# Kernel tuning notes

Hardware: AMD Instinct MI355X
Metric: run time of the kernel (lower is better)

The kernel has to match this reference:

```python
import jax, jax.numpy as jnp
import numpy as np

N, D = 8192, 128

def setup_inputs() -> dict:
    key = jax.random.key(0)
    kF, kS = jax.random.split(key)
    F = jax.random.normal(kF, (N, D), dtype=jnp.float32)
    S = jax.random.uniform(kS, (N, N), dtype=jnp.float32)
    return {"F": F, "S": S, "t": 1, "T": 10}

def reference(F, S, t, T):
    # Pairwise squared euclidean distances via Gram trick:
    # D_ij = ||f_i||^2 + ||f_j||^2 - 2 f_i . f_j  (same math as norm(F[:,None]-F)^2)
    sq = jnp.sum(F * F, axis=1)                      # [N]
    dist2 = sq[:, None] + sq[None, :] - 2.0 * (F @ F.T)  # [N, N]
    # select=False: loss = sum over i of sum_j dist2[i,j] * S[i,j]
    loss = jnp.sum(dist2 * S)
    return loss
```

## Files before the change

kernel.cpp:

```cpp
#include <hip/hip_runtime.h>

#define NN 8192
#define DD 128
#define BM 128
#define NTILE (NN / BM)

typedef __attribute__((ext_vector_type(8))) short bf16x8;
typedef __attribute__((ext_vector_type(4))) float f32x4;

__device__ __forceinline__ ushort f2bf(float x) {
    unsigned u = __float_as_uint(x);
    unsigned r = u + 0x7FFFu + ((u >> 16) & 1u);
    return (ushort)(r >> 16);
}

__device__ __forceinline__ void async16(void* lds, const void* g) {
    __builtin_amdgcn_global_load_lds(
        (const __attribute__((address_space(1))) unsigned*)g,
        (__attribute__((address_space(3))) unsigned*)lds, 16, 0, 0);
}
__device__ __forceinline__ void async4(void* lds, const void* g) {
    __builtin_amdgcn_global_load_lds(
        (const __attribute__((address_space(1))) unsigned*)g,
        (__attribute__((address_space(3))) unsigned*)lds, 4, 0, 0);
}

__global__ void prep_kernel(const float* __restrict__ F, ushort* __restrict__ Fbf,
                            float* __restrict__ sq, int doFbf) {
    int gtid = blockIdx.x * blockDim.x + threadIdx.x;
    int row  = gtid >> 6;
    int lane = threadIdx.x & 63;
    const float2 v = *(const float2*)(F + (size_t)row * DD + lane * 2);
    if (doFbf)
        ((ushort2*)(Fbf + (size_t)row * DD))[lane] = make_ushort2(f2bf(v.x), f2bf(v.y));
    float s = v.x * v.x + v.y * v.y;
    #pragma unroll
    for (int off = 32; off > 0; off >>= 1) s += __shfl_down(s, off);
    if (lane == 0) sq[row] = s;
}

template <int FAST>
__global__ __launch_bounds__(256, 2) void tile_kernel(
        const ushort* __restrict__ Fbf, const float* __restrict__ F,
        const float* __restrict__ S, const float* __restrict__ sq,
        float* __restrict__ partials) {
    __shared__ ushort lI[BM * DD];
    __shared__ ushort lJ[BM * DD];
    __shared__ float  sqi[BM];
    __shared__ float  sqj[BM];
    __shared__ float  red[4];

    const int bi = blockIdx.y, bj = blockIdx.x;
    const int gi = bi * BM, gj = bj * BM;
    const int tid = threadIdx.x;
    const int w = tid >> 6, l = tid & 63;

    if (FAST) {
        #pragma unroll
        for (int it = 0; it < 8; ++it) {
            const int chunk = it * 4 + w;
            const int row = chunk * 4 + (l >> 4);
            const int inb = (l & 15) * 16;
            const int src = inb ^ ((row & 7) << 4);
            async16((char*)lI + chunk * 1024, (const char*)(Fbf + (size_t)(gi + row) * DD) + src);
            async16((char*)lJ + chunk * 1024, (const char*)(Fbf + (size_t)(gj + row) * DD) + src);
        }
        {
            float* dstb = (w < 2 ? sqi : sqj) + (w & 1) * 64;
            const float* srcb = sq + (w < 2 ? gi : gj) + (w & 1) * 64 + l;
            async4(dstb, srcb);
        }
    } else {
        const int r0 = tid >> 5;
        const int c4 = (tid & 31) * 4;
        #pragma unroll
        for (int it = 0; it < 16; ++it) {
            const int row = it * 8 + r0;
            const float4 va = *(const float4*)(F + (size_t)(gi + row) * DD + c4);
            const float4 vb = *(const float4*)(F + (size_t)(gj + row) * DD + c4);
            int byte = row * 256 + c4 * 2;
            byte ^= (row & 7) << 4;
            *(ushort4*)((char*)lI + byte) =
                make_ushort4(f2bf(va.x), f2bf(va.y), f2bf(va.z), f2bf(va.w));
            *(ushort4*)((char*)lJ + byte) =
                make_ushort4(f2bf(vb.x), f2bf(vb.y), f2bf(vb.z), f2bf(vb.w));
        }
        if (tid < 128) sqi[tid] = sq[gi + tid];
        else           sqj[tid - 128] = sq[gj + tid - 128];
    }
    __syncthreads();

    const int fr = l & 15;
    const int g  = l >> 4;
    const int jw = w * 32;

    float4 sv0[8], sv1[8];
    #pragma unroll
    for (int ct = 0; ct < 8; ++ct) {
        const float* srow = S + (size_t)(gi + ct * 16 + fr) * NN + gj + jw + g * 4;
        sv0[ct] = *(const float4*)(srow);
        sv1[ct] = *(const float4*)(srow + 16);
    }

    bf16x8 afrag[2][4];
    #pragma unroll
    for (int kk = 0; kk < 4; ++kk) {
        {
            const int row = jw + fr;
            int byte = row * 256 + kk * 64 + g * 16;
            byte ^= (row & 7) << 4;
            afrag[0][kk] = *(const bf16x8*)((const char*)lJ + byte);
        }
        {
            const int row = jw + 16 + fr;
            int byte = row * 256 + kk * 64 + g * 16;
            byte ^= (row & 7) << 4;
            afrag[1][kk] = *(const bf16x8*)((const char*)lJ + byte);
        }
    }

    f32x4 acc[2][8];
    #pragma unroll
    for (int ct = 0; ct < 8; ++ct) {
        acc[0][ct] = (f32x4){0.f, 0.f, 0.f, 0.f};
        acc[1][ct] = (f32x4){0.f, 0.f, 0.f, 0.f};
    }

    #pragma unroll
    for (int ct = 0; ct < 8; ++ct) {
        #pragma unroll
        for (int kk = 0; kk < 4; ++kk) {
            const int row = ct * 16 + fr;
            int byte = row * 256 + kk * 64 + g * 16;
            byte ^= (row & 7) << 4;
            const bf16x8 bfrag = *(const bf16x8*)((const char*)lI + byte);
            acc[0][ct] = __builtin_amdgcn_mfma_f32_16x16x32_bf16(
                afrag[0][kk], bfrag, acc[0][ct], 0, 0, 0);
            acc[1][ct] = __builtin_amdgcn_mfma_f32_16x16x32_bf16(
                afrag[1][kk], bfrag, acc[1][ct], 0, 0, 0);
        }
    }

    const float4 sj0 = *(const float4*)(sqj + jw + g * 4);
    const float4 sj1 = *(const float4*)(sqj + jw + 16 + g * 4);
    float part = 0.f;
    #pragma unroll
    for (int ct = 0; ct < 8; ++ct) {
        const float si = sqi[ct * 16 + fr];
        const float4 s0 = sv0[ct], s1 = sv1[ct];
        part += s0.x * (si + sj0.x - 2.f * acc[0][ct][0]);
        part += s0.y * (si + sj0.y - 2.f * acc[0][ct][1]);
        part += s0.z * (si + sj0.z - 2.f * acc[0][ct][2]);
        part += s0.w * (si + sj0.w - 2.f * acc[0][ct][3]);
        part += s1.x * (si + sj1.x - 2.f * acc[1][ct][0]);
        part += s1.y * (si + sj1.y - 2.f * acc[1][ct][1]);
        part += s1.z * (si + sj1.z - 2.f * acc[1][ct][2]);
        part += s1.w * (si + sj1.w - 2.f * acc[1][ct][3]);
    }

    #pragma unroll
    for (int off = 32; off > 0; off >>= 1) part += __shfl_down(part, off);
    if (l == 0) red[w] = part;
    __syncthreads();
    if (tid == 0)
        partials[blockIdx.y * gridDim.x + blockIdx.x] = (red[0] + red[1]) + (red[2] + red[3]);
}

__global__ void reduce_kernel(const float* __restrict__ partials, float* __restrict__ out) {
    __shared__ float sm[256];
    const int t = threadIdx.x;
    float s = 0.f;
    for (int i = t; i < NTILE * NTILE; i += 256) s += partials[i];
    sm[t] = s;
    __syncthreads();
    for (int off = 128; off > 0; off >>= 1) {
        if (t < off) sm[t] += sm[t + off];
        __syncthreads();
    }
    if (t == 0) out[0] = sm[0];
}

extern "C" void kernel_launch(void* const* d_in, const int* in_sizes, int n_in,
                              void* d_out, int out_size, void* d_ws, size_t ws_size,
                              hipStream_t stream) {
    const float* F = (const float*)d_in[0];
    const float* S = (const float*)d_in[1];
    float* sq       = (float*)d_ws;
    float* partials = sq + NN;
    ushort* Fbf     = (ushort*)((char*)d_ws + 48 * 1024);
    float* out      = (float*)d_out;

    const size_t need = 48 * 1024 + (size_t)NN * DD * 2 + 256;
    const int fast = (ws_size >= need) ? 1 : 0;

    prep_kernel<<<NN / 4, 256, 0, stream>>>(F, Fbf, sq, fast);
    dim3 grid(NTILE, NTILE);
    if (fast)
        tile_kernel<1><<<grid, 256, 0, stream>>>(Fbf, F, S, sq, partials);
    else
        tile_kernel<0><<<grid, 256, 0, stream>>>(Fbf, F, S, sq, partials);
    reduce_kernel<<<1, 256, 0, stream>>>(partials, out);
}
```

Baseline: 69.13 us.

## Persistent row-block loop with double-buffered J tiles and fused final reduction

Replaces the one-tile-per-block grid with 256 blocks of 512 threads, each looping over 16 column tiles for a fixed row block. The I tile stays resident in LDS while the next J tile (via async global-to-LDS loads) and its S values are prefetched into double buffers during the MFMA work on the current tile. The separate reduce kernel is dropped in favour of an atomic-counter last-block reduction, removing one launch. The cost is more registers and LDS per block, hand-tuned waitcnt values that must match the number of outstanding loads, and only 256 blocks to spread across the CUs.

```diff
diff --git a/kernel.cpp b/kernel.cpp
--- a/kernel.cpp
+++ b/kernel.cpp
@@ -3,6 +3,7 @@
 #define NN 8192
 #define DD 128
 #define BM 128
+#define NT 16
 #define NTILE (NN / BM)
 
 typedef __attribute__((ext_vector_type(8))) short bf16x8;
@@ -19,14 +20,10 @@
         (const __attribute__((address_space(1))) unsigned*)g,
         (__attribute__((address_space(3))) unsigned*)lds, 16, 0, 0);
 }
-__device__ __forceinline__ void async4(void* lds, const void* g) {
-    __builtin_amdgcn_global_load_lds(
-        (const __attribute__((address_space(1))) unsigned*)g,
-        (__attribute__((address_space(3))) unsigned*)lds, 4, 0, 0);
-}
 
 __global__ void prep_kernel(const float* __restrict__ F, ushort* __restrict__ Fbf,
-                            float* __restrict__ sq, int doFbf) {
+                            float* __restrict__ sq, int* counter, int doFbf) {
+    if (blockIdx.x == 0 && threadIdx.x == 0 && counter) *counter = 0;
     int gtid = blockIdx.x * blockDim.x + threadIdx.x;
     int row  = gtid >> 6;
     int lane = threadIdx.x & 63;
@@ -39,11 +36,143 @@
     if (lane == 0) sq[row] = s;
 }
 
-template <int FAST>
-__global__ __launch_bounds__(256, 2) void tile_kernel(
-        const ushort* __restrict__ Fbf, const float* __restrict__ F,
-        const float* __restrict__ S, const float* __restrict__ sq,
-        float* __restrict__ partials) {
+#define BODY(T, SVC, SJC, SVN, SJN, RBUF, WBUF)                               \
+  {                                                                           \
+    const int t_ = (T);                                                       \
+    if (t_ < NT - 1) {                                                        \
+      const int jr0 = jg0 + (t_ + 1) * BM;                                    \
+      _Pragma("unroll")                                                       \
+      for (int it = 0; it < 4; ++it) {                                        \
+        const int c = it * 8 + w;                                             \
+        const int row = c * 4 + (l >> 4);                                     \
+        const int src = ((l & 15) * 16) ^ ((row & 7) << 4);                   \
+        async16((char*)(WBUF) + c * 1024,                                     \
+                (const char*)(Fbf + (size_t)(jr0 + row) * DD) + src);         \
+      }                                                                       \
+      __builtin_amdgcn_sched_barrier(0);                                      \
+      const float* sb_ = sbase + jr0;                                         \
+      _Pragma("unroll")                                                       \
+      for (int ct = 0; ct < 8; ++ct)                                          \
+        SVN[ct] = *(const float4*)(sb_ + (size_t)ct * 16 * NN);               \
+      SJN = *(const float4*)(sq + jr0 + jcol);                                \
+      __builtin_amdgcn_sched_barrier(0);                                      \
+    }                                                                         \
+    bf16x8 af[4];                                                             \
+    {                                                                         \
+      const int row = jw + fr;                                                \
+      const int sw = (row & 7) << 4;                                          \
+      _Pragma("unroll")                                                       \
+      for (int kk = 0; kk < 4; ++kk)                                          \
+        af[kk] = *(const bf16x8*)((const char*)RBUF + row * 256 +             \
+                                  ((kk * 64 + g * 16) ^ sw));                 \
+    }                                                                         \
+    f32x4 acc[8];                                                             \
+    _Pragma("unroll")                                                         \
+    for (int ct = 0; ct < 8; ++ct) acc[ct] = (f32x4){0.f, 0.f, 0.f, 0.f};     \
+    _Pragma("unroll")                                                         \
+    for (int ct = 0; ct < 8; ++ct) {                                          \
+      const int row = ct * 16 + fr;                                           \
+      const int sw = (row & 7) << 4;                                          \
+      _Pragma("unroll")                                                       \
+      for (int kk = 0; kk < 4; ++kk) {                                        \
+        const bf16x8 bf_ = *(const bf16x8*)((const char*)lI + row * 256 +     \
+                                            ((kk * 64 + g * 16) ^ sw));       \
+        acc[ct] = __builtin_amdgcn_mfma_f32_16x16x32_bf16(af[kk], bf_,        \
+                                                          acc[ct], 0, 0, 0);  \
+      }                                                                       \
+    }                                                                         \
+    _Pragma("unroll")                                                         \
+    for (int ct = 0; ct < 8; ++ct) {                                          \
+      const float4 s4 = SVC[ct];                                              \
+      const float c0 = si[ct] + SJC.x, c1 = si[ct] + SJC.y,                   \
+                  c2 = si[ct] + SJC.z, c3 = si[ct] + SJC.w;                   \
+      part0 += s4.x * (c0 - 2.f * acc[ct][0]);                                \
+      part1 += s4.y * (c1 - 2.f * acc[ct][1]);                                \
+      part0 += s4.z * (c2 - 2.f * acc[ct][2]);                                \
+      part1 += s4.w * (c3 - 2.f * acc[ct][3]);                                \
+    }                                                                         \
+    if (t_ < NT - 1) {                                                        \
+      asm volatile("s_waitcnt vmcnt(9)" ::: "memory");                        \
+      __builtin_amdgcn_sched_barrier(0);                                      \
+      __builtin_amdgcn_s_barrier();                                           \
+    }                                                                         \
+  }
+
+__global__ __launch_bounds__(512, 2) void tile_loop_kernel(
+        const ushort* __restrict__ Fbf, const float* __restrict__ S,
+        const float* __restrict__ sq, float* __restrict__ partials,
+        int* __restrict__ counter, float* __restrict__ out) {
+    __shared__ ushort lI[BM * DD];
+    __shared__ ushort lJ0[BM * DD];
+    __shared__ ushort lJ1[BM * DD];
+    __shared__ float  red[8];
+
+    const int bi  = blockIdx.y;
+    const int jg  = blockIdx.x;
+    const int gi  = bi * BM;
+    const int jg0 = jg * (NT * BM);
+    const int tid = threadIdx.x;
+    const int w = tid >> 6, l = tid & 63;
+    const int fr = l & 15, g = l >> 4;
+    const int jw = w * 16;
+    const int jcol = jw + g * 4;
+
+    #pragma unroll
+    for (int it = 0; it < 4; ++it) {
+        const int c = it * 8 + w;
+        const int row = c * 4 + (l >> 4);
+        const int src = ((l & 15) * 16) ^ ((row & 7) << 4);
+        async16((char*)lI  + c * 1024, (const char*)(Fbf + (size_t)(gi  + row) * DD) + src);
+        async16((char*)lJ0 + c * 1024, (const char*)(Fbf + (size_t)(jg0 + row) * DD) + src);
+    }
+    __builtin_amdgcn_sched_barrier(0);
+
+    float si[8];
+    #pragma unroll
+    for (int ct = 0; ct < 8; ++ct) si[ct] = sq[gi + ct * 16 + fr];
+
+    const float* sbase = S + (size_t)(gi + fr) * NN + jcol;
+    float4 svA[8], svB[8], sjA, sjB;
+    #pragma unroll
+    for (int ct = 0; ct < 8; ++ct)
+        svA[ct] = *(const float4*)(sbase + jg0 + (size_t)ct * 16 * NN);
+    sjA = *(const float4*)(sq + jg0 + jcol);
+    __builtin_amdgcn_sched_barrier(0);
+    asm volatile("s_waitcnt vmcnt(17)" ::: "memory");
+    __builtin_amdgcn_sched_barrier(0);
+    __builtin_amdgcn_s_barrier();
+
+    float part0 = 0.f, part1 = 0.f;
+
+    for (int tt = 0; tt < NT; tt += 2) {
+        BODY(tt,     svA, sjA, svB, sjB, lJ0, lJ1);
+        BODY(tt + 1, svB, sjB, svA, sjA, lJ1, lJ0);
+    }
+
+    float part = part0 + part1;
+    #pragma unroll
+    for (int off = 32; off > 0; off >>= 1) part += __shfl_down(part, off);
+    if (l == 0) red[w] = part;
+    __syncthreads();
+    if (tid == 0) {
+        float r = ((red[0] + red[1]) + (red[2] + red[3])) +
+                  ((red[4] + red[5]) + (red[6] + red[7]));
+        const int bx = blockIdx.y * gridDim.x + blockIdx.x;
+        partials[bx] = r;
+        __threadfence();
+        if (atomicAdd(counter, 1) == 255) {
+            __threadfence();
+            volatile const float* vp = partials;
+            float tot = 0.f;
+            for (int i = 0; i < 256; ++i) tot += vp[i];
+            out[0] = tot;
+        }
+    }
+}
+
+__global__ __launch_bounds__(256, 2) void tile_fb_kernel(
+        const float* __restrict__ F, const float* __restrict__ S,
+        const float* __restrict__ sq, float* __restrict__ partials) {
     __shared__ ushort lI[BM * DD];
     __shared__ ushort lJ[BM * DD];
     __shared__ float  sqi[BM];
@@ -55,39 +184,22 @@
     const int tid = threadIdx.x;
     const int w = tid >> 6, l = tid & 63;
 
-    if (FAST) {
-        #pragma unroll
-        for (int it = 0; it < 8; ++it) {
-            const int chunk = it * 4 + w;
-            const int row = chunk * 4 + (l >> 4);
-            const int inb = (l & 15) * 16;
-            const int src = inb ^ ((row & 7) << 4);
-            async16((char*)lI + chunk * 1024, (const char*)(Fbf + (size_t)(gi + row) * DD) + src);
-            async16((char*)lJ + chunk * 1024, (const char*)(Fbf + (size_t)(gj + row) * DD) + src);
-        }
-        {
-            float* dstb = (w < 2 ? sqi : sqj) + (w & 1) * 64;
-            const float* srcb = sq + (w < 2 ? gi : gj) + (w & 1) * 64 + l;
-            async4(dstb, srcb);
-        }
-    } else {
-        const int r0 = tid >> 5;
-        const int c4 = (tid & 31) * 4;
-        #pragma unroll
-        for (int it = 0; it < 16; ++it) {
-            const int row = it * 8 + r0;
-            const float4 va = *(const float4*)(F + (size_t)(gi + row) * DD + c4);
-            const float4 vb = *(const float4*)(F + (size_t)(gj + row) * DD + c4);
-            int byte = row * 256 + c4 * 2;
-            byte ^= (row & 7) << 4;
-            *(ushort4*)((char*)lI + byte) =
-                make_ushort4(f2bf(va.x), f2bf(va.y), f2bf(va.z), f2bf(va.w));
-            *(ushort4*)((char*)lJ + byte) =
-                make_ushort4(f2bf(vb.x), f2bf(vb.y), f2bf(vb.z), f2bf(vb.w));
-        }
-        if (tid < 128) sqi[tid] = sq[gi + tid];
-        else           sqj[tid - 128] = sq[gj + tid - 128];
-    }
+    const int r0 = tid >> 5;
+    const int c4 = (tid & 31) * 4;
+    #pragma unroll
+    for (int it = 0; it < 16; ++it) {
+        const int row = it * 8 + r0;
+        const float4 va = *(const float4*)(F + (size_t)(gi + row) * DD + c4);
+        const float4 vb = *(const float4*)(F + (size_t)(gj + row) * DD + c4);
+        int byte = row * 256 + c4 * 2;
+        byte ^= (row & 7) << 4;
+        *(ushort4*)((char*)lI + byte) =
+            make_ushort4(f2bf(va.x), f2bf(va.y), f2bf(va.z), f2bf(va.w));
+        *(ushort4*)((char*)lJ + byte) =
+            make_ushort4(f2bf(vb.x), f2bf(vb.y), f2bf(vb.z), f2bf(vb.w));
+    }
+    if (tid < 128) sqi[tid] = sq[gi + tid];
+    else           sqj[tid - 128] = sq[gj + tid - 128];
     __syncthreads();
 
     const int fr = l & 15;
@@ -105,18 +217,12 @@
     bf16x8 afrag[2][4];
     #pragma unroll
     for (int kk = 0; kk < 4; ++kk) {
-        {
-            const int row = jw + fr;
-            int byte = row * 256 + kk * 64 + g * 16;
-            byte ^= (row & 7) << 4;
-            afrag[0][kk] = *(const bf16x8*)((const char*)lJ + byte);
-        }
-        {
-            const int row = jw + 16 + fr;
-            int byte = row * 256 + kk * 64 + g * 16;
-            byte ^= (row & 7) << 4;
-            afrag[1][kk] = *(const bf16x8*)((const char*)lJ + byte);
-        }
+        int row = jw + fr;
+        int byte = row * 256 + kk * 64 + g * 16; byte ^= (row & 7) << 4;
+        afrag[0][kk] = *(const bf16x8*)((const char*)lJ + byte);
+        row = jw + 16 + fr;
+        byte = row * 256 + kk * 64 + g * 16; byte ^= (row & 7) << 4;
+        afrag[1][kk] = *(const bf16x8*)((const char*)lJ + byte);
     }
 
     f32x4 acc[2][8];
@@ -125,19 +231,15 @@
         acc[0][ct] = (f32x4){0.f, 0.f, 0.f, 0.f};
         acc[1][ct] = (f32x4){0.f, 0.f, 0.f, 0.f};
     }
-
     #pragma unroll
     for (int ct = 0; ct < 8; ++ct) {
         #pragma unroll
         for (int kk = 0; kk < 4; ++kk) {
             const int row = ct * 16 + fr;
-            int byte = row * 256 + kk * 64 + g * 16;
-            byte ^= (row & 7) << 4;
+            int byte = row * 256 + kk * 64 + g * 16; byte ^= (row & 7) << 4;
             const bf16x8 bfrag = *(const bf16x8*)((const char*)lI + byte);
-            acc[0][ct] = __builtin_amdgcn_mfma_f32_16x16x32_bf16(
-                afrag[0][kk], bfrag, acc[0][ct], 0, 0, 0);
-            acc[1][ct] = __builtin_amdgcn_mfma_f32_16x16x32_bf16(
-                afrag[1][kk], bfrag, acc[1][ct], 0, 0, 0);
+            acc[0][ct] = __builtin_amdgcn_mfma_f32_16x16x32_bf16(afrag[0][kk], bfrag, acc[0][ct], 0, 0, 0);
+            acc[1][ct] = __builtin_amdgcn_mfma_f32_16x16x32_bf16(afrag[1][kk], bfrag, acc[1][ct], 0, 0, 0);
         }
     }
 
@@ -146,16 +248,16 @@
     float part = 0.f;
     #pragma unroll
     for (int ct = 0; ct < 8; ++ct) {
-        const float si = sqi[ct * 16 + fr];
+        const float sic = sqi[ct * 16 + fr];
         const float4 s0 = sv0[ct], s1 = sv1[ct];
-        part += s0.x * (si + sj0.x - 2.f * acc[0][ct][0]);
-        part += s0.y * (si + sj0.y - 2.f * acc[0][ct][1]);
-        part += s0.z * (si + sj0.z - 2.f * acc[0][ct][2]);
-        part += s0.w * (si + sj0.w - 2.f * acc[0][ct][3]);
-        part += s1.x * (si + sj1.x - 2.f * acc[1][ct][0]);
-        part += s1.y * (si + sj1.y - 2.f * acc[1][ct][1]);
-        part += s1.z * (si + sj1.z - 2.f * acc[1][ct][2]);
-        part += s1.w * (si + sj1.w - 2.f * acc[1][ct][3]);
+        part += s0.x * (sic + sj0.x - 2.f * acc[0][ct][0]);
+        part += s0.y * (sic + sj0.y - 2.f * acc[0][ct][1]);
+        part += s0.z * (sic + sj0.z - 2.f * acc[0][ct][2]);
+        part += s0.w * (sic + sj0.w - 2.f * acc[0][ct][3]);
+        part += s1.x * (sic + sj1.x - 2.f * acc[1][ct][0]);
+        part += s1.y * (sic + sj1.y - 2.f * acc[1][ct][1]);
+        part += s1.z * (sic + sj1.z - 2.f * acc[1][ct][2]);
+        part += s1.w * (sic + sj1.w - 2.f * acc[1][ct][3]);
     }
 
     #pragma unroll
@@ -185,19 +287,20 @@
                               hipStream_t stream) {
     const float* F = (const float*)d_in[0];
     const float* S = (const float*)d_in[1];
-    float* sq       = (float*)d_ws;
-    float* partials = sq + NN;
-    ushort* Fbf     = (ushort*)((char*)d_ws + 48 * 1024);
-    float* out      = (float*)d_out;
-
-    const size_t need = 48 * 1024 + (size_t)NN * DD * 2 + 256;
+    float* sq        = (float*)d_ws;
+    float* partials  = sq + NN;
+    int*   counter   = (int*)((char*)d_ws + 33792);
+    ushort* Fbf      = (ushort*)((char*)d_ws + 49152);
+    float* out       = (float*)d_out;
+
+    const size_t need = 49152 + (size_t)NN * DD * 2 + 256;
     const int fast = (ws_size >= need) ? 1 : 0;
 
-    prep_kernel<<<NN / 4, 256, 0, stream>>>(F, Fbf, sq, fast);
-    dim3 grid(NTILE, NTILE);
-    if (fast)
-        tile_kernel<1><<<grid, 256, 0, stream>>>(Fbf, F, S, sq, partials);
-    else
-        tile_kernel<0><<<grid, 256, 0, stream>>>(Fbf, F, S, sq, partials);
-    reduce_kernel<<<1, 256, 0, stream>>>(partials, out);
-}
+    prep_kernel<<<NN / 4, 256, 0, stream>>>(F, Fbf, sq, fast ? counter : nullptr, fast);
+    if (fast) {
+        tile_loop_kernel<<<dim3(4, 64), 512, 0, stream>>>(Fbf, S, sq, partials, counter, out);
+    } else {
+        tile_fb_kernel<<<dim3(NTILE, NTILE), 256, 0, stream>>>(F, S, sq, partials);
+        reduce_kernel<<<1, 256, 0, stream>>>(partials, out);
+    }
+}
```

Result: slower. 94.09 us (+36.1%).
